# Kernel optimization log

Hardware: AMD Instinct MI355X
Metric: run time of the kernel (lower is better)

Reference implementation:

```python
import jax, jax.numpy as jnp
import numpy as np
from jax import lax

# Model dims (match init_kwargs config)
HID = 2048      # hidden_size
NH = 64         # num_heads
P = 64          # head_dim
N = 128         # ssm_state_size
G = 1           # n_groups
CS = 256        # chunk_size
K = 4           # conv kernel
D_INNER = NH * P                  # 4096
CONV_DIM = D_INNER + 2 * G * N    # 4352
PROJ = D_INNER + CONV_DIM + NH    # 8512
EPS = 1e-5
BATCH, SEQ = 2, 2048


def setup_inputs() -> dict:
    key = jax.random.key(0)
    ks = jax.random.split(key, 8)
    hidden_states = jax.random.normal(ks[0], (BATCH, SEQ, HID), dtype=jnp.float32)
    W_in = jax.random.normal(ks[1], (PROJ, HID), dtype=jnp.float32) * 0.02
    conv_w = jax.random.normal(ks[2], (CONV_DIM, 1, K), dtype=jnp.float32) * 0.2
    conv_b = jax.random.normal(ks[3], (CONV_DIM,), dtype=jnp.float32) * 0.02
    # dt_bias initialized like inv-softplus of dt in [1e-3, 1e-1]
    dt = jnp.exp(jax.random.uniform(ks[4], (NH,)) * (np.log(0.1) - np.log(0.001)) + np.log(0.001))
    dt_bias = (dt + jnp.log(-jnp.expm1(-dt))).astype(jnp.float32)
    A_log = jnp.log(jnp.arange(1, NH + 1, dtype=jnp.float32))
    D_param = jnp.ones((NH,), dtype=jnp.float32)
    norm_w = jnp.ones((D_INNER,), dtype=jnp.float32)
    W_out = jax.random.normal(ks[5], (HID, D_INNER), dtype=jnp.float32) * 0.02
    return {"hidden_states": hidden_states, "W_in": W_in, "conv_w": conv_w,
            "conv_b": conv_b, "dt_bias": dt_bias, "A_log": A_log,
            "D_param": D_param, "norm_w": norm_w, "W_out": W_out}


def _segsum(x):
    # x: (..., c) -> (..., c, c); seg[i, j] = sum_{j < k <= i} x_k (diag 0), -inf above diag
    T = x.shape[-1]
    xc = jnp.cumsum(x, axis=-1)
    seg = xc[..., :, None] - xc[..., None, :]
    mask = jnp.tril(jnp.ones((T, T), dtype=bool))
    return jnp.where(mask, seg, -jnp.inf)


def _mamba2_forward(hidden_states, W_in, conv_w, conv_b, dt_bias, A_log, D_param, norm_w, W_out):
    B_, L_ = hidden_states.shape[:2]
    proj = hidden_states @ W_in.T                           # (b, l, PROJ)
    z = proj[..., :D_INNER]                                 # gate
    xBC = proj[..., D_INNER:D_INNER + CONV_DIM]
    dt = proj[..., D_INNER + CONV_DIM:]                     # (b, l, NH)

    # depthwise causal conv1d + silu
    xc = lax.conv_general_dilated(
        jnp.transpose(xBC, (0, 2, 1)), conv_w,
        window_strides=(1,), padding=[(K - 1, 0)],
        feature_group_count=CONV_DIM)                        # (b, CONV_DIM, l)
    xc = xc + conv_b[None, :, None]
    xBC = jax.nn.silu(jnp.transpose(xc, (0, 2, 1)))          # (b, l, CONV_DIM)

    x = xBC[..., :D_INNER].reshape(B_, L_, NH, P)
    Bm = xBC[..., D_INNER:D_INNER + G * N].reshape(B_, L_, G, N)
    Cm = xBC[..., D_INNER + G * N:].reshape(B_, L_, G, N)

    dt = jax.nn.softplus(dt + dt_bias)                       # (b, l, NH)
    A = -jnp.exp(A_log)                                      # (NH,)

    Bh = jnp.repeat(Bm, NH // G, axis=2)                     # (b, l, h, n)
    Ch = jnp.repeat(Cm, NH // G, axis=2)

    # ---- chunked SSD scan ----
    nc = L_ // CS
    x_dt = (x * dt[..., None]).reshape(B_, nc, CS, NH, P)    # (b, c, s, h, p)
    B_c = Bh.reshape(B_, nc, CS, NH, N)
    C_c = Ch.reshape(B_, nc, CS, NH, N)
    dA = jnp.transpose((dt * A).reshape(B_, nc, CS, NH), (0, 3, 1, 2))  # (b, h, c, s)
    A_cum = jnp.cumsum(dA, axis=-1)                          # (b, h, c, s)

    Lmat = jnp.exp(_segsum(dA))                              # (b, h, c, s, s)
    Y_diag = jnp.einsum('bclhn,bcshn,bhcls,bcshp->bclhp', C_c, B_c, Lmat, x_dt)

    decay_states = jnp.exp(A_cum[..., -1:] - A_cum)          # (b, h, c, s)
    states = jnp.einsum('bclhn,bhcl,bclhp->bchpn', B_c, decay_states, x_dt)

    da_last = A_cum[..., -1]                                 # (b, h, c)

    def step(prev, inp):
        s_k, d_k = inp                                       # (b,h,p,n), (b,h)
        new = prev * jnp.exp(d_k)[..., None, None] + s_k
        return new, prev

    _, prev_states = lax.scan(step, jnp.zeros((B_, NH, P, N), dtype=x.dtype),
                              (jnp.transpose(states, (1, 0, 2, 3, 4)),
                               jnp.transpose(da_last, (2, 0, 1))))
    prev_states = jnp.transpose(prev_states, (1, 2, 0, 3, 4))  # (b, h, c, p, n)

    Y_off = jnp.einsum('bclhn,bhcpn,bhcl->bclhp', C_c, prev_states, jnp.exp(A_cum))

    y = (Y_diag + Y_off).reshape(B_, L_, NH, P) + D_param[None, None, :, None] * x
    y = y.reshape(B_, L_, D_INNER)

    # gated grouped RMSNorm (norm_before_gate=False): norm(y * silu(z)) * w
    g = y * jax.nn.silu(z)
    gs = D_INNER // G
    gr = g.reshape(B_, L_, G, gs)
    var = jnp.mean(gr * gr, axis=-1, keepdims=True)
    gn = (gr * lax.rsqrt(var + EPS)).reshape(B_, L_, D_INNER) * norm_w

    return gn @ W_out.T                                      # (b, l, HID)


def reference(hidden_states, W_in, conv_w, conv_b, dt_bias, A_log, D_param, norm_w, W_out):
    return _mamba2_forward(hidden_states, W_in, conv_w, conv_b, dt_bias, A_log, D_param, norm_w, W_out)
```

## Files before the change

kernel.cpp:

```cpp
#include <hip/hip_runtime.h>

#define SEQLEN 2048
#define NHEADS 64
#define PDIM 64
#define NSTATE 128
#define CSIZE 256
#define NCHUNK 8
#define DINNER 4096
#define CONVD 4352
#define PROJD 8512

using s8v = __attribute__((ext_vector_type(8))) short;
using f4v = __attribute__((ext_vector_type(4))) float;
using bf8v = __attribute__((ext_vector_type(8))) __bf16;

__device__ __forceinline__ short f2bf(float x) {
  union { float f; unsigned u; } t; t.f = x;
  unsigned r = t.u + 0x7FFFu + ((t.u >> 16) & 1u);
  return (short)(r >> 16);
}
__device__ __forceinline__ float bf2f(short s) {
  union { unsigned u; float f; } t;
  t.u = ((unsigned)(unsigned short)s) << 16;
  return t.f;
}

__device__ __forceinline__ f4v mfma_bf16(s8v a, s8v b, f4v c) {
  return __builtin_amdgcn_mfma_f32_16x16x32_bf16(
      __builtin_bit_cast(bf8v, a), __builtin_bit_cast(bf8v, b), c, 0, 0, 0);
}

__device__ __forceinline__ void gll16(const void* g, void* l) {
  __builtin_amdgcn_global_load_lds(
      (const __attribute__((address_space(1))) unsigned*)g,
      (__attribute__((address_space(3))) unsigned*)l, 16, 0, 0);
}

__global__ __launch_bounds__(256) void cast_bf16_kernel(
    const float* __restrict__ in, short* __restrict__ out, int n4) {
  int i = blockIdx.x * 256 + threadIdx.x;
  if (i < n4) {
    float4 v = ((const float4*)in)[i];
    short4 o;
    o.x = f2bf(v.x); o.y = f2bf(v.y); o.z = f2bf(v.z); o.w = f2bf(v.w);
    ((short4*)out)[i] = o;
  }
}

__global__ __launch_bounds__(256) void gemm1_kernel(
    const short* __restrict__ A, const short* __restrict__ B,
    short* __restrict__ z, short* __restrict__ xbc, float* __restrict__ dtb) {
  const int K = 2048;
  const int tn0 = blockIdx.x * 128;
  const int tm0 = blockIdx.y * 128;
  __shared__ short As[128 * 32];
  __shared__ short Bs[128 * 32];
  __shared__ short Cs[128 * 136];
  const int tid = threadIdx.x;
  const int lane = tid & 63, wid = tid >> 6;
  const int wm = (wid >> 1) * 64, wn = (wid & 1) * 64;
  const int lr = lane & 15, q = lane >> 4;
  f4v acc[4][4];
  for (int i = 0; i < 4; i++)
    for (int j = 0; j < 4; j++)
      for (int r = 0; r < 4; r++) acc[i][j][r] = 0.f;

  for (int k0 = 0; k0 < K; k0 += 32) {
    __syncthreads();
    for (int it = 0; it < 2; it++) {
      int ci = it * 256 + tid;
      int row = ci >> 2, col8 = (ci & 3) << 3;
      gll16(&A[(size_t)(tm0 + row) * K + k0 + col8], &As[ci * 8]);
      gll16(&B[(size_t)(tn0 + row) * K + k0 + col8], &Bs[ci * 8]);
    }
    __syncthreads();
    s8v af[4], bfr[4];
    for (int i = 0; i < 4; i++) af[i]  = *(const s8v*)&As[(wm + i * 16 + lr) * 32 + q * 8];
    for (int j = 0; j < 4; j++) bfr[j] = *(const s8v*)&Bs[(wn + j * 16 + lr) * 32 + q * 8];
    for (int i = 0; i < 4; i++)
      for (int j = 0; j < 4; j++)
        acc[i][j] = mfma_bf16(af[i], bfr[j], acc[i][j]);
  }

  if (tn0 < 8448) {
    for (int i = 0; i < 4; i++)
      for (int j = 0; j < 4; j++)
        for (int r = 0; r < 4; r++)
          Cs[(wm + i * 16 + q * 4 + r) * 136 + wn + j * 16 + lr] = f2bf(acc[i][j][r]);
    __syncthreads();
    short* outp; int rowstride, colbase;
    if (tn0 < DINNER) { outp = z;   rowstride = DINNER; colbase = tn0; }
    else              { outp = xbc; rowstride = CONVD;  colbase = tn0 - DINNER; }
    for (int ps = 0; ps < 8; ps++) {
      int r = ps * 16 + (tid >> 4);
      int c8 = (tid & 15) * 8;
      s8v v = *(const s8v*)&Cs[r * 136 + c8];
      *(s8v*)&outp[(size_t)(tm0 + r) * rowstride + colbase + c8] = v;
    }
  } else {
    for (int i = 0; i < 4; i++)
      for (int j = 0; j < 4; j++) {
        int c0 = tn0 + wn + j * 16 + lr;
        if (c0 < PROJD)
          for (int r = 0; r < 4; r++)
            dtb[(size_t)(tm0 + wm + i * 16 + q * 4 + r) * NHEADS + (c0 - 8448)] =
                acc[i][j][r];
      }
  }
}

__global__ __launch_bounds__(256) void gemm_nt_bf16(
    const short* __restrict__ A, const short* __restrict__ B,
    float* __restrict__ C, int M, int N, int K) {
  const int tn0 = blockIdx.x * 128;
  const int tm0 = blockIdx.y * 128;
  __shared__ short As[128 * 32];
  __shared__ short Bs[128 * 32];
  const int tid = threadIdx.x;
  const int lane = tid & 63, wid = tid >> 6;
  const int wm = (wid >> 1) * 64, wn = (wid & 1) * 64;
  const int lr = lane & 15, q = lane >> 4;
  f4v acc[4][4];
  for (int i = 0; i < 4; i++)
    for (int j = 0; j < 4; j++)
      for (int r = 0; r < 4; r++) acc[i][j][r] = 0.f;

  for (int k0 = 0; k0 < K; k0 += 32) {
    __syncthreads();
    for (int it = 0; it < 2; it++) {
      int ci = it * 256 + tid;
      int row = ci >> 2, col8 = (ci & 3) << 3;
      gll16(&A[(size_t)(tm0 + row) * K + k0 + col8], &As[ci * 8]);
      gll16(&B[(size_t)(tn0 + row) * K + k0 + col8], &Bs[ci * 8]);
    }
    __syncthreads();
    s8v af[4], bfr[4];
    for (int i = 0; i < 4; i++) af[i]  = *(const s8v*)&As[(wm + i * 16 + lr) * 32 + q * 8];
    for (int j = 0; j < 4; j++) bfr[j] = *(const s8v*)&Bs[(wn + j * 16 + lr) * 32 + q * 8];
    for (int i = 0; i < 4; i++)
      for (int j = 0; j < 4; j++)
        acc[i][j] = mfma_bf16(af[i], bfr[j], acc[i][j]);
  }
  for (int i = 0; i < 4; i++)
    for (int j = 0; j < 4; j++) {
      int r0 = tm0 + wm + i * 16 + q * 4;
      int c0 = tn0 + wn + j * 16 + lr;
      for (int r = 0; r < 4; r++)
        C[(size_t)(r0 + r) * N + c0] = acc[i][j][r];
    }
}

__global__ __launch_bounds__(256) void conv_silu_kernel(
    const short* __restrict__ xbc, const float* __restrict__ conv_w,
    const float* __restrict__ conv_b, short* __restrict__ xBCc) {
  int cc = blockIdx.x * 256 + threadIdx.x;
  int bl = blockIdx.y;
  int b = bl >> 11, l = bl & 2047;
  float4 wv = *(const float4*)&conv_w[cc * 4];
  float wk[4] = {wv.x, wv.y, wv.z, wv.w};
  float acc = conv_b[cc];
  const short* pbase = xbc + (size_t)(b * SEQLEN) * CONVD + cc;
#pragma unroll
  for (int k = 0; k < 4; k++) {
    int ls = l - 3 + k;
    if (ls >= 0) acc += bf2f(pbase[(size_t)ls * CONVD]) * wk[k];
  }
  float sv = acc / (1.f + expf(-acc));
  xBCc[(size_t)bl * CONVD + cc] = f2bf(sv);
}

__global__ __launch_bounds__(256) void dt_kernel(
    float* __restrict__ dtb, const float* __restrict__ dt_bias) {
  int idx = blockIdx.x * 256 + threadIdx.x;
  int hh = idx & 63;
  float v = dtb[idx] + dt_bias[hh];
  dtb[idx] = (v > 20.f) ? v : log1pf(expf(v));
}

__global__ __launch_bounds__(256) void ssd_states_kernel(
    const short* __restrict__ xBCc, const float* __restrict__ dtp,
    const float* __restrict__ A_log, short* __restrict__ states,
    float* __restrict__ da_last) {
  const int blk = blockIdx.x;
  const int h = blk & 63, cc = (blk >> 6) & 7, b = blk >> 9;
  const int tid = threadIdx.x;
  __shared__ float dt_s[CSIZE], Acum[CSIZE], w_s[CSIZE];
  __shared__ float xw[64][64];
  __shared__ float Bt[64][NSTATE];
  const size_t row0 = (size_t)(b * SEQLEN + cc * CSIZE);
  dt_s[tid] = dtp[(row0 + tid) * NHEADS + h];
  __syncthreads();
  if (tid == 0) {
    float Aval = -expf(A_log[h]);
    float s = 0.f;
    for (int i = 0; i < CSIZE; i++) { s += dt_s[i]; Acum[i] = s * Aval; }
    da_last[(size_t)(b * NHEADS + h) * NCHUNK + cc] = Acum[CSIZE - 1];
  }
  __syncthreads();
  float total = Acum[CSIZE - 1];
  w_s[tid] = dt_s[tid] * expf(total - Acum[tid]);
  float acc[4][8];
  for (int a = 0; a < 4; a++) for (int j = 0; j < 8; j++) acc[a][j] = 0.f;
  const int pi = (tid & 15) * 4, ni = (tid >> 4) * 8;
  for (int lt = 0; lt < 4; lt++) {
    __syncthreads();
    for (int i = 0; i < 4; i++) {
      int idx = tid + i * 256;
      int r = idx >> 4, c4 = (idx & 15) << 2;
      short4 v = *(const short4*)&xBCc[(row0 + lt * 64 + r) * CONVD + h * PDIM + c4];
      float wl = w_s[lt * 64 + r];
      xw[r][c4 + 0] = bf2f(v.x) * wl;
      xw[r][c4 + 1] = bf2f(v.y) * wl;
      xw[r][c4 + 2] = bf2f(v.z) * wl;
      xw[r][c4 + 3] = bf2f(v.w) * wl;
    }
    for (int i = 0; i < 8; i++) {
      int idx = tid + i * 256;
      int r = idx >> 5, c4 = (idx & 31) << 2;
      short4 v = *(const short4*)&xBCc[(row0 + lt * 64 + r) * CONVD + DINNER + c4];
      Bt[r][c4 + 0] = bf2f(v.x);
      Bt[r][c4 + 1] = bf2f(v.y);
      Bt[r][c4 + 2] = bf2f(v.z);
      Bt[r][c4 + 3] = bf2f(v.w);
    }
    __syncthreads();
    for (int l = 0; l < 64; l++) {
      float4 xv = *(const float4*)&xw[l][pi];
      float4 b0 = *(const float4*)&Bt[l][ni];
      float4 b1 = *(const float4*)&Bt[l][ni + 4];
      float xa[4] = {xv.x, xv.y, xv.z, xv.w};
      float bb[8] = {b0.x, b0.y, b0.z, b0.w, b1.x, b1.y, b1.z, b1.w};
      for (int a = 0; a < 4; a++)
        for (int j = 0; j < 8; j++)
          acc[a][j] += xa[a] * bb[j];
    }
  }
  const size_t sbase = (((size_t)b * NCHUNK + cc) * NHEADS + h) * (PDIM * NSTATE);
  for (int a = 0; a < 4; a++) {
    short o[8];
    for (int j = 0; j < 8; j++) o[j] = f2bf(acc[a][j]);
    *(s8v*)&states[sbase + (size_t)(pi + a) * NSTATE + ni] = *(const s8v*)o;
  }
}

__global__ __launch_bounds__(256) void scan_kernel(
    short* __restrict__ states, const float* __restrict__ da_last) {
  const int bh = blockIdx.x;
  const int b = bh >> 6, h = bh & 63;
  const int tid = threadIdx.x;
  float prev[32];
  for (int i = 0; i < 32; i++) prev[i] = 0.f;
  for (int c = 0; c < NCHUNK; c++) {
    const size_t base = (((size_t)b * NCHUNK + c) * NHEADS + h) * (PDIM * NSTATE);
    const float d = expf(da_last[(size_t)bh * NCHUNK + c]);
    for (int i = 0; i < 32; i++) {
      size_t e = base + tid + i * 256;
      float s = bf2f(states[e]);
      states[e] = f2bf(prev[i]);
      prev[i] = prev[i] * d + s;
    }
  }
}

__global__ __launch_bounds__(256) void ssd_y_kernel(
    const short* __restrict__ xBCc, const float* __restrict__ dtp,
    const float* __restrict__ A_log, const float* __restrict__ D_param,
    const short* __restrict__ prevs, short* __restrict__ y) {
  const int blk = blockIdx.x;
  const int h = blk & 63, cc = (blk >> 6) & 7, b = blk >> 9;
  const int tid = threadIdx.x;
  const int lane = tid & 63, w = tid >> 6;
  const int lr = lane & 15, q = lane >> 4;
  __shared__ float dt_s[CSIZE];
  __shared__ float Acum[CSIZE];
  __shared__ short C_s[64][136];
  __shared__ short BP_s[64][136];
  __shared__ short xdtT[64][72];
  __shared__ short Mt[64][72];
  const size_t row0 = (size_t)(b * SEQLEN + cc * CSIZE);
  dt_s[tid] = dtp[(row0 + tid) * NHEADS + h];
  __syncthreads();
  if (tid == 0) {
    float Aval = -expf(A_log[h]);
    float s = 0.f;
    for (int i = 0; i < CSIZE; i++) { s += dt_s[i]; Acum[i] = s * Aval; }
  }
  const float Dh = D_param[h];
  const size_t prevbase = (((size_t)b * NCHUNK + cc) * NHEADS + h) * (PDIM * NSTATE);
  const int wl0 = w * 16;

  for (int lt = 0; lt < 4; lt++) {
    __syncthreads();
    for (int i = 0; i < 4; i++) {
      int idx = tid + i * 256;
      int r = idx >> 4, c8 = (idx & 15) << 3;
      *(s8v*)&C_s[r][c8] =
          *(const s8v*)&xBCc[(row0 + lt * 64 + r) * CONVD + DINNER + NSTATE + c8];
      *(s8v*)&BP_s[r][c8] = *(const s8v*)&prevs[prevbase + (size_t)r * NSTATE + c8];
    }
    __syncthreads();
    f4v acc[4];
    for (int j = 0; j < 4; j++) for (int r = 0; r < 4; r++) acc[j][r] = 0.f;
    for (int ks = 0; ks < 4; ks++) {
      s8v a = *(const s8v*)&C_s[wl0 + lr][ks * 32 + q * 8];
      for (int j = 0; j < 4; j++) {
        s8v bb = *(const s8v*)&BP_s[j * 16 + lr][ks * 32 + q * 8];
        acc[j] = mfma_bf16(a, bb, acc[j]);
      }
    }
    for (int r = 0; r < 4; r++) {
      float e = __expf(Acum[lt * 64 + wl0 + q * 4 + r]);
      for (int j = 0; j < 4; j++) acc[j][r] *= e;
    }
    for (int st = 0; st <= lt; st++) {
      __syncthreads();
      for (int i = 0; i < 4; i++) {
        int idx = tid + i * 256;
        int r = idx >> 4, c8 = (idx & 15) << 3;
        *(s8v*)&BP_s[r][c8] =
            *(const s8v*)&xBCc[(row0 + st * 64 + r) * CONVD + DINNER + c8];
      }
      for (int i = 0; i < 4; i++) {
        int idx = tid + i * 256;
        int r = idx >> 4, c4 = (idx & 15) << 2;
        float dtv = dt_s[st * 64 + r];
        short4 v = *(const short4*)&xBCc[(row0 + st * 64 + r) * CONVD + h * PDIM + c4];
        xdtT[c4 + 0][r] = f2bf(bf2f(v.x) * dtv);
        xdtT[c4 + 1][r] = f2bf(bf2f(v.y) * dtv);
        xdtT[c4 + 2][r] = f2bf(bf2f(v.z) * dtv);
        xdtT[c4 + 3][r] = f2bf(bf2f(v.w) * dtv);
      }
      __syncthreads();
      f4v sacc[4];
      for (int j = 0; j < 4; j++) for (int r = 0; r < 4; r++) sacc[j][r] = 0.f;
      for (int ks = 0; ks < 4; ks++) {
        s8v a = *(const s8v*)&C_s[wl0 + lr][ks * 32 + q * 8];
        for (int j = 0; j < 4; j++) {
          s8v bb = *(const s8v*)&BP_s[j * 16 + lr][ks * 32 + q * 8];
          sacc[j] = mfma_bf16(a, bb, sacc[j]);
        }
      }
      int lbase = lt * 64 + wl0 + q * 4;
      for (int j = 0; j < 4; j++) {
        int sg = st * 64 + j * 16 + lr;
        for (int r = 0; r < 4; r++) {
          int ll = lbase + r;
          float m = (sg <= ll) ? sacc[j][r] * __expf(Acum[ll] - Acum[sg]) : 0.f;
          Mt[wl0 + q * 4 + r][j * 16 + lr] = f2bf(m);
        }
      }
      __syncthreads();
      for (int ss2 = 0; ss2 < 2; ss2++) {
        s8v a = *(const s8v*)&Mt[wl0 + lr][ss2 * 32 + q * 8];
        for (int j = 0; j < 4; j++) {
          s8v bb = *(const s8v*)&xdtT[j * 16 + lr][ss2 * 32 + q * 8];
          acc[j] = mfma_bf16(a, bb, acc[j]);
        }
      }
    }
    for (int j = 0; j < 4; j++)
      for (int r = 0; r < 4; r++) {
        int lrow = wl0 + q * 4 + r;
        int ll = lt * 64 + lrow;
        int p = j * 16 + lr;
        float xv = bf2f(xBCc[(row0 + ll) * CONVD + h * PDIM + p]);
        Mt[lrow][p] = f2bf(acc[j][r] + Dh * xv);
      }
    __syncthreads();
    for (int ps = 0; ps < 2; ps++) {
      int r = ps * 32 + (tid >> 3);
      int c8 = (tid & 7) * 8;
      s8v v = *(const s8v*)&Mt[r][c8];
      *(s8v*)&y[(row0 + lt * 64 + r) * DINNER + h * PDIM + c8] = v;
    }
  }
}

__global__ __launch_bounds__(256) void norm_kernel(
    const short* __restrict__ y, const short* __restrict__ z,
    const float* __restrict__ norm_w, short* __restrict__ g) {
  int bl = blockIdx.x, tid = threadIdx.x;
  const short4* yrow = (const short4*)(y + (size_t)bl * DINNER);
  const short4* zrow = (const short4*)(z + (size_t)bl * DINNER);
  float gv[16];
  float ss = 0.f;
  for (int i = 0; i < 4; i++) {
    short4 yv = yrow[tid + i * 256];
    short4 zv = zrow[tid + i * 256];
    float zf[4] = {bf2f(zv.x), bf2f(zv.y), bf2f(zv.z), bf2f(zv.w)};
    float yf[4] = {bf2f(yv.x), bf2f(yv.y), bf2f(yv.z), bf2f(yv.w)};
    for (int t = 0; t < 4; t++) {
      float gg = yf[t] * (zf[t] / (1.f + expf(-zf[t])));
      gv[i * 4 + t] = gg;
      ss += gg * gg;
    }
  }
  for (int off = 32; off > 0; off >>= 1) ss += __shfl_down(ss, off);
  __shared__ float red[4];
  __shared__ float rsS;
  if ((tid & 63) == 0) red[tid >> 6] = ss;
  __syncthreads();
  if (tid == 0) rsS = rsqrtf((red[0] + red[1] + red[2] + red[3]) * (1.f / 4096.f) + 1e-5f);
  __syncthreads();
  float rs = rsS;
  for (int i = 0; i < 4; i++) {
    int j4 = (tid + i * 256) * 4;
    float4 nw = *(const float4*)&norm_w[j4];
    short4 o;
    o.x = f2bf(gv[i * 4 + 0] * rs * nw.x);
    o.y = f2bf(gv[i * 4 + 1] * rs * nw.y);
    o.z = f2bf(gv[i * 4 + 2] * rs * nw.z);
    o.w = f2bf(gv[i * 4 + 3] * rs * nw.w);
    *(short4*)&g[(size_t)bl * DINNER + j4] = o;
  }
}

extern "C" void kernel_launch(void* const* d_in, const int* in_sizes, int n_in,
                              void* d_out, int out_size, void* d_ws, size_t ws_size,
                              hipStream_t stream) {
  const float* hidden  = (const float*)d_in[0];
  const float* W_in    = (const float*)d_in[1];
  const float* conv_w  = (const float*)d_in[2];
  const float* conv_b  = (const float*)d_in[3];
  const float* dt_bias = (const float*)d_in[4];
  const float* A_log   = (const float*)d_in[5];
  const float* D_param = (const float*)d_in[6];
  const float* norm_w  = (const float*)d_in[7];
  const float* W_out   = (const float*)d_in[8];
  float* out = (float*)d_out;

  char* ws = (char*)d_ws;
  short* z_bf  = (short*)(ws + 0);
  float* dtb   = (float*)(ws + 33554432);
  float* da_l  = (float*)(ws + 34603008);
  short* xbc_pre = (short*)(ws + 34607104);
  short* y_bf    = (short*)(ws + 34607104);
  short* hid_bf  = (short*)(ws + 70258688);
  short* win_bf  = (short*)(ws + 87035904);
  short* xBCc    = (short*)(ws + 70258688);
  short* states  = (short*)(ws + 105910272);
  short* g_bf    = (short*)(ws + 70258688);
  short* wout_bf = (short*)(ws + 105910272);
  if (ws_size < (size_t)122687488) return;

  cast_bf16_kernel<<<8192, 256, 0, stream>>>(hidden, hid_bf, 2097152);
  cast_bf16_kernel<<<17024, 256, 0, stream>>>(W_in, win_bf, 4358144);

  gemm1_kernel<<<dim3(67, 32), 256, 0, stream>>>(hid_bf, win_bf, z_bf, xbc_pre, dtb);

  conv_silu_kernel<<<dim3(17, 4096), 256, 0, stream>>>(xbc_pre, conv_w, conv_b, xBCc);
  dt_kernel<<<1024, 256, 0, stream>>>(dtb, dt_bias);

  ssd_states_kernel<<<1024, 256, 0, stream>>>(xBCc, dtb, A_log, states, da_l);
  scan_kernel<<<128, 256, 0, stream>>>(states, da_l);
  ssd_y_kernel<<<1024, 256, 0, stream>>>(xBCc, dtb, A_log, D_param, states, y_bf);

  norm_kernel<<<4096, 256, 0, stream>>>(y_bf, z_bf, norm_w, g_bf);
  cast_bf16_kernel<<<8192, 256, 0, stream>>>(W_out, wout_bf, 2097152);

  gemm_nt_bf16<<<dim3(16, 32), 256, 0, stream>>>(g_bf, wout_bf, out, 4096, 2048, 4096);
}
```

Measured before the change: 776.4 us.

## Swizzle GEMM LDS, group block order, shrink epilogue LDS, split scan

Both bf16 GEMMs now XOR-swizzle the 16-byte column groups in LDS to cut bank conflicts on fragment reads. They also map a 1D grid onto panels of 4 row-tiles so neighbouring blocks share B tiles in L2, and declare launch bounds of 4 blocks per CU. gemm1 reuses the A/B LDS for a half-height epilogue staging buffer written in two passes, which lowers LDS use per block at the cost of extra barriers. The scan kernel is split into 4 slices per (batch, head) so it launches 512 blocks instead of 128, giving more parallelism to a memory-bound pass.

```diff
diff --git a/kernel.cpp b/kernel.cpp
--- a/kernel.cpp
+++ b/kernel.cpp
@@ -47,19 +47,24 @@
   }
 }
 
-__global__ __launch_bounds__(256) void gemm1_kernel(
+__global__ __launch_bounds__(256, 4) void gemm1_kernel(
     const short* __restrict__ A, const short* __restrict__ B,
     short* __restrict__ z, short* __restrict__ xbc, float* __restrict__ dtb) {
   const int K = 2048;
-  const int tn0 = blockIdx.x * 128;
-  const int tm0 = blockIdx.y * 128;
-  __shared__ short As[128 * 32];
-  __shared__ short Bs[128 * 32];
-  __shared__ short Cs[128 * 136];
+  const int bid = blockIdx.x;
+  const int panel = bid / (67 * 4), rem = bid % (67 * 4);
+  const int bx = rem >> 2, by = panel * 4 + (rem & 3);
+  const int tn0 = bx * 128, tm0 = by * 128;
+  __shared__ alignas(16) short lds[8704];
+  short* As = lds;
+  short* Bs = lds + 4096;
+  short* Cs = lds;
   const int tid = threadIdx.x;
   const int lane = tid & 63, wid = tid >> 6;
   const int wm = (wid >> 1) * 64, wn = (wid & 1) * 64;
   const int lr = lane & 15, q = lane >> 4;
+  const int fA = (lr & 3) ^ ((lr >> 2) & 3);
+  const int qs = (q ^ fA) * 8;
   f4v acc[4][4];
   for (int i = 0; i < 4; i++)
     for (int j = 0; j < 4; j++)
@@ -69,33 +74,40 @@
     __syncthreads();
     for (int it = 0; it < 2; it++) {
       int ci = it * 256 + tid;
-      int row = ci >> 2, col8 = (ci & 3) << 3;
-      gll16(&A[(size_t)(tm0 + row) * K + k0 + col8], &As[ci * 8]);
-      gll16(&B[(size_t)(tn0 + row) * K + k0 + col8], &Bs[ci * 8]);
+      int row = ci >> 2;
+      int cg = ((ci & 3) ^ (row & 3) ^ ((row >> 2) & 3)) << 3;
+      gll16(&A[(size_t)(tm0 + row) * K + k0 + cg], &As[ci * 8]);
+      gll16(&B[(size_t)(tn0 + row) * K + k0 + cg], &Bs[ci * 8]);
     }
     __syncthreads();
     s8v af[4], bfr[4];
-    for (int i = 0; i < 4; i++) af[i]  = *(const s8v*)&As[(wm + i * 16 + lr) * 32 + q * 8];
-    for (int j = 0; j < 4; j++) bfr[j] = *(const s8v*)&Bs[(wn + j * 16 + lr) * 32 + q * 8];
+    for (int i = 0; i < 4; i++) af[i]  = *(const s8v*)&As[(wm + i * 16 + lr) * 32 + qs];
+    for (int j = 0; j < 4; j++) bfr[j] = *(const s8v*)&Bs[(wn + j * 16 + lr) * 32 + qs];
     for (int i = 0; i < 4; i++)
       for (int j = 0; j < 4; j++)
         acc[i][j] = mfma_bf16(af[i], bfr[j], acc[i][j]);
   }
+  __syncthreads();
 
   if (tn0 < 8448) {
-    for (int i = 0; i < 4; i++)
-      for (int j = 0; j < 4; j++)
-        for (int r = 0; r < 4; r++)
-          Cs[(wm + i * 16 + q * 4 + r) * 136 + wn + j * 16 + lr] = f2bf(acc[i][j][r]);
-    __syncthreads();
     short* outp; int rowstride, colbase;
     if (tn0 < DINNER) { outp = z;   rowstride = DINNER; colbase = tn0; }
     else              { outp = xbc; rowstride = CONVD;  colbase = tn0 - DINNER; }
-    for (int ps = 0; ps < 8; ps++) {
-      int r = ps * 16 + (tid >> 4);
-      int c8 = (tid & 15) * 8;
-      s8v v = *(const s8v*)&Cs[r * 136 + c8];
-      *(s8v*)&outp[(size_t)(tm0 + r) * rowstride + colbase + c8] = v;
+    for (int hh = 0; hh < 2; hh++) {
+      if ((wid >> 1) == hh) {
+        for (int i = 0; i < 4; i++)
+          for (int j = 0; j < 4; j++)
+            for (int r = 0; r < 4; r++)
+              Cs[(i * 16 + q * 4 + r) * 136 + wn + j * 16 + lr] = f2bf(acc[i][j][r]);
+      }
+      __syncthreads();
+      for (int ps = 0; ps < 4; ps++) {
+        int idx = ps * 256 + tid;
+        int r = idx >> 4, c8 = (idx & 15) * 8;
+        s8v v = *(const s8v*)&Cs[r * 136 + c8];
+        *(s8v*)&outp[(size_t)(tm0 + hh * 64 + r) * rowstride + colbase + c8] = v;
+      }
+      __syncthreads();
     }
   } else {
     for (int i = 0; i < 4; i++)
@@ -109,17 +121,22 @@
   }
 }
 
-__global__ __launch_bounds__(256) void gemm_nt_bf16(
+__global__ __launch_bounds__(256, 4) void gemm_nt_bf16(
     const short* __restrict__ A, const short* __restrict__ B,
     float* __restrict__ C, int M, int N, int K) {
-  const int tn0 = blockIdx.x * 128;
-  const int tm0 = blockIdx.y * 128;
-  __shared__ short As[128 * 32];
-  __shared__ short Bs[128 * 32];
+  const int nbx = N >> 7;
+  const int bid = blockIdx.x;
+  const int panel = bid / (nbx * 4), rem = bid % (nbx * 4);
+  const int bx = rem >> 2, by = panel * 4 + (rem & 3);
+  const int tn0 = bx * 128, tm0 = by * 128;
+  __shared__ alignas(16) short As[128 * 32];
+  __shared__ alignas(16) short Bs[128 * 32];
   const int tid = threadIdx.x;
   const int lane = tid & 63, wid = tid >> 6;
   const int wm = (wid >> 1) * 64, wn = (wid & 1) * 64;
   const int lr = lane & 15, q = lane >> 4;
+  const int fA = (lr & 3) ^ ((lr >> 2) & 3);
+  const int qs = (q ^ fA) * 8;
   f4v acc[4][4];
   for (int i = 0; i < 4; i++)
     for (int j = 0; j < 4; j++)
@@ -129,14 +146,15 @@
     __syncthreads();
     for (int it = 0; it < 2; it++) {
       int ci = it * 256 + tid;
-      int row = ci >> 2, col8 = (ci & 3) << 3;
-      gll16(&A[(size_t)(tm0 + row) * K + k0 + col8], &As[ci * 8]);
-      gll16(&B[(size_t)(tn0 + row) * K + k0 + col8], &Bs[ci * 8]);
+      int row = ci >> 2;
+      int cg = ((ci & 3) ^ (row & 3) ^ ((row >> 2) & 3)) << 3;
+      gll16(&A[(size_t)(tm0 + row) * K + k0 + cg], &As[ci * 8]);
+      gll16(&B[(size_t)(tn0 + row) * K + k0 + cg], &Bs[ci * 8]);
     }
     __syncthreads();
     s8v af[4], bfr[4];
-    for (int i = 0; i < 4; i++) af[i]  = *(const s8v*)&As[(wm + i * 16 + lr) * 32 + q * 8];
-    for (int j = 0; j < 4; j++) bfr[j] = *(const s8v*)&Bs[(wn + j * 16 + lr) * 32 + q * 8];
+    for (int i = 0; i < 4; i++) af[i]  = *(const s8v*)&As[(wm + i * 16 + lr) * 32 + qs];
+    for (int j = 0; j < 4; j++) bfr[j] = *(const s8v*)&Bs[(wn + j * 16 + lr) * 32 + qs];
     for (int i = 0; i < 4; i++)
       for (int j = 0; j < 4; j++)
         acc[i][j] = mfma_bf16(af[i], bfr[j], acc[i][j]);
@@ -245,15 +263,16 @@
 
 __global__ __launch_bounds__(256) void scan_kernel(
     short* __restrict__ states, const float* __restrict__ da_last) {
-  const int bh = blockIdx.x;
+  const int bh = blockIdx.x >> 2, sl = blockIdx.x & 3;
   const int b = bh >> 6, h = bh & 63;
   const int tid = threadIdx.x;
-  float prev[32];
-  for (int i = 0; i < 32; i++) prev[i] = 0.f;
+  float prev[8];
+  for (int i = 0; i < 8; i++) prev[i] = 0.f;
   for (int c = 0; c < NCHUNK; c++) {
-    const size_t base = (((size_t)b * NCHUNK + c) * NHEADS + h) * (PDIM * NSTATE);
+    const size_t base = (((size_t)b * NCHUNK + c) * NHEADS + h) * (PDIM * NSTATE)
+                      + sl * 2048;
     const float d = expf(da_last[(size_t)bh * NCHUNK + c]);
-    for (int i = 0; i < 32; i++) {
+    for (int i = 0; i < 8; i++) {
       size_t e = base + tid + i * 256;
       float s = bf2f(states[e]);
       states[e] = f2bf(prev[i]);
@@ -446,17 +465,17 @@
   cast_bf16_kernel<<<8192, 256, 0, stream>>>(hidden, hid_bf, 2097152);
   cast_bf16_kernel<<<17024, 256, 0, stream>>>(W_in, win_bf, 4358144);
 
-  gemm1_kernel<<<dim3(67, 32), 256, 0, stream>>>(hid_bf, win_bf, z_bf, xbc_pre, dtb);
+  gemm1_kernel<<<2144, 256, 0, stream>>>(hid_bf, win_bf, z_bf, xbc_pre, dtb);
 
   conv_silu_kernel<<<dim3(17, 4096), 256, 0, stream>>>(xbc_pre, conv_w, conv_b, xBCc);
   dt_kernel<<<1024, 256, 0, stream>>>(dtb, dt_bias);
 
   ssd_states_kernel<<<1024, 256, 0, stream>>>(xBCc, dtb, A_log, states, da_l);
-  scan_kernel<<<128, 256, 0, stream>>>(states, da_l);
+  scan_kernel<<<512, 256, 0, stream>>>(states, da_l);
   ssd_y_kernel<<<1024, 256, 0, stream>>>(xBCc, dtb, A_log, D_param, states, y_bf);
 
   norm_kernel<<<4096, 256, 0, stream>>>(y_bf, z_bf, norm_w, g_bf);
   cast_bf16_kernel<<<8192, 256, 0, stream>>>(W_out, wout_bf, 2097152);
 
-  gemm_nt_bf16<<<dim3(16, 32), 256, 0, stream>>>(g_bf, wout_bf, out, 4096, 2048, 4096);
-}
+  gemm_nt_bf16<<<512, 256, 0, stream>>>(g_bf, wout_bf, out, 4096, 2048, 4096);
+}
```

Result: faster. 698.0 us (-10.1%).
